# Optimization experiments

Hardware: AMD Instinct MI355X
Metric: run time of the kernel (lower is better)

## Reference

```python
import jax, jax.numpy as jnp
import numpy as np

TAU = 0.05
EPS = 1e-12


def _l2_normalize(x):
    # F.normalize(p=2): x / max(||x||, eps)
    n = jnp.sqrt(jnp.sum(x * x, axis=-1, keepdims=True))
    return x / jnp.maximum(n, EPS)


def _masked_lse(sim, mask):
    # logsumexp over axis -1 restricted to mask; rows with empty mask are
    # masked out downstream (has_pos), so we guard the log to stay finite.
    neg_inf = jnp.finfo(sim.dtype).min
    mx = jnp.max(jnp.where(mask, sim, neg_inf), axis=-1)
    mx_safe = jnp.where(mx > neg_inf / 2, mx, 0.0)
    s = jnp.sum(jnp.where(mask, jnp.exp(sim - mx_safe[:, None]), 0.0), axis=-1)
    return mx_safe + jnp.log(jnp.where(s > 0, s, 1.0))


def setup_inputs() -> dict:
    key = jax.random.key(0)
    k1, k2, k3, k4 = jax.random.split(key, 4)
    B, S, D = 64, 128, 256
    return {
        "logits": jax.random.normal(k1, (B, S, D), dtype=jnp.float32),
        "labels": jax.random.normal(k2, (B, S, D), dtype=jnp.float32),
        "pad_mask": jax.random.randint(k3, (B, S), 0, 2, dtype=jnp.int32),
        "ad_idxs": jax.random.randint(k4, (B, S), 0, 500, dtype=jnp.int32),
    }


def reference(logits, labels, pad_mask, ad_idxs):
    B, S, D = logits.shape
    q = _l2_normalize(logits.reshape(B * S, D))
    k = _l2_normalize(labels.reshape(B * S, D))
    valid = pad_mask.reshape(B * S).astype(bool)
    ad = ad_idxs.reshape(B * S)

    sim = jnp.einsum("nd,md->nm", q, k) / TAU          # [N, N]
    pair_valid = valid[None, :] & valid[:, None]
    pos_mask = (ad[None, :] == ad[:, None]) & pair_valid

    pos_lse = _masked_lse(sim, pos_mask)
    all_lse = _masked_lse(sim, pair_valid)
    has_pos = jnp.any(pos_mask, axis=-1)

    loss_per_row = -(pos_lse - all_lse)
    # mean over rows with at least one positive (== loss_per_row[has_pos].mean())
    cnt = jnp.sum(has_pos.astype(sim.dtype))
    loss = jnp.sum(jnp.where(has_pos, loss_per_row, 0.0)) / jnp.maximum(cnt, 1.0)
    return loss
```

## Files before the change

### kernel.cpp

```cpp
#include <hip/hip_runtime.h>
#include <hip/hip_bf16.h>
#include <hip/hip_fp8.h>
#include <math.h>

typedef float f32x4 __attribute__((ext_vector_type(4)));
typedef int   i32x4 __attribute__((ext_vector_type(4)));
typedef int   v8i   __attribute__((ext_vector_type(8)));

constexpr int Nn = 8192;
constexpr int Dd = 256;
constexpr float LOG2E     = 1.4426950408889634f;
constexpr float SIM_SCALE = 20.0f * LOG2E;
constexpr float SIM_BIAS  = -20.0f * LOG2E;
constexpr int   SCALE1    = 0x7F7F7F7F;

typedef __attribute__((address_space(1))) const unsigned int gu32;
typedef __attribute__((address_space(3))) unsigned int lu32;
__device__ __forceinline__ void gload16(const unsigned char* g, unsigned char* l) {
  __builtin_amdgcn_global_load_lds((gu32*)(uintptr_t)g, (lu32*)(uintptr_t)l, 16, 0, 0);
}

__global__ __launch_bounds__(256) void prep_kernel(const float* __restrict__ logits,
                                                   const float* __restrict__ labels,
                                                   const int* __restrict__ pad,
                                                   unsigned char* __restrict__ qb,
                                                   unsigned char* __restrict__ kb,
                                                   float* __restrict__ cbias,
                                                   float* __restrict__ g_all,
                                                   float* __restrict__ g_pos) {
  const int j = blockIdx.x * 256 + threadIdx.x;
  if (j < Nn) {
    cbias[j] = pad[j] ? SIM_BIAS : -1e30f;
    g_all[j] = 0.0f;
    g_pos[j] = 0.0f;
  }

  const int gw   = (blockIdx.x * 256 + threadIdx.x) >> 6;
  const int lane = threadIdx.x & 63;
  const float* src;
  unsigned char* dst;
  int row;
  if (gw < Nn) { src = logits; dst = qb; row = gw; }
  else         { src = labels; dst = kb; row = gw - Nn; }

  const float4 v = *reinterpret_cast<const float4*>(src + (size_t)row * Dd + lane * 4);
  float ss = v.x * v.x + v.y * v.y + v.z * v.z + v.w * v.w;
#pragma unroll
  for (int m = 32; m >= 1; m >>= 1) ss += __shfl_xor(ss, m);
  const float scale = 1.0f / fmaxf(sqrtf(ss), 1e-12f);

  const __hip_fp8_e4m3 e0(v.x * scale);
  const __hip_fp8_e4m3 e1(v.y * scale);
  const __hip_fp8_e4m3 e2(v.z * scale);
  const __hip_fp8_e4m3 e3(v.w * scale);
  const unsigned int packed = (unsigned int)e0.__x |
                              ((unsigned int)e1.__x << 8) |
                              ((unsigned int)e2.__x << 16) |
                              ((unsigned int)e3.__x << 24);
  reinterpret_cast<unsigned int*>(dst + (size_t)row * Dd)[lane] = packed;
}

__global__ __launch_bounds__(256, 2) void gemm_lse_kernel(const unsigned char* __restrict__ qb,
                                                          const unsigned char* __restrict__ kb,
                                                          const float* __restrict__ cbias,
                                                          const int* __restrict__ ad,
                                                          float* __restrict__ g_all,
                                                          float* __restrict__ g_pos) {
  __shared__ unsigned char smem[65536];

  const int tid  = threadIdx.x;
  const int lane = tid & 63;
  const int w    = tid >> 6;
  const int wrow = (w >> 1) * 64;
  const int wcolL = (w & 1) * 64;
  const int lq   = lane & 15;
  const int qd   = lane >> 4;
  const int rowBase = blockIdx.x * 128;
  const int colBase = blockIdx.y * 1024;

  const int srl = lane >> 3;
  const int cg  = (lane & 7) ^ srl;
  const unsigned char* gA0 = qb + (size_t)(rowBase + w * 32 + srl) * Dd + cg * 16;
  const unsigned char* gB0 = kb + (size_t)(colBase + w * 32 + srl) * Dd + cg * 16;

#pragma unroll
  for (int kk = 0; kk < 2; ++kk)
#pragma unroll
    for (int i = 0; i < 4; ++i)
      gload16(gA0 + (size_t)i * 8 * Dd + kk * 128,
              &smem[kk * 16384 + (w * 32 + i * 8) * 128]);
#pragma unroll
  for (int i = 0; i < 4; ++i)
    gload16(gB0 + (size_t)i * 8 * Dd, &smem[32768 + (w * 32 + i * 8) * 128]);

  int rowAd[4][4];
#pragma unroll
  for (int mt = 0; mt < 4; ++mt)
#pragma unroll
    for (int r = 0; r < 4; ++r)
      rowAd[mt][r] = ad[rowBase + wrow + mt * 16 + qd * 4 + r];

  float apA[4][4], apP[4][4];
#pragma unroll
  for (int mt = 0; mt < 4; ++mt)
#pragma unroll
    for (int r = 0; r < 4; ++r) {
      apA[mt][r] = 0.f;
      apP[mt][r] = 0.f;
    }

  __syncthreads();

  const int g0 = qd << 1;
  const int sl = lq & 7;
  const int s0 = (g0 ^ sl) << 4;
  const int s1 = ((g0 + 1) ^ sl) << 4;

  v8i afReg[2][4];
#pragma unroll
  for (int kk = 0; kk < 2; ++kk) {
    const unsigned char* Ah = &smem[kk * 16384];
#pragma unroll
    for (int mt = 0; mt < 4; ++mt) {
      const int rb = (wrow + mt * 16 + lq) * 128;
      i32x4* ph = reinterpret_cast<i32x4*>(&afReg[kk][mt]);
      ph[0] = *reinterpret_cast<const i32x4*>(&Ah[rb + s0]);
      ph[1] = *reinterpret_cast<const i32x4*>(&Ah[rb + s1]);
    }
  }

  const f32x4 CZ = (f32x4){0.f, 0.f, 0.f, 0.f};
  f32x4 c[4][4];
  float colB[4];
  int colAd[4];

  for (int ct = 0; ct < 8; ++ct) {
    {
      const unsigned char* g = gB0 + (size_t)(ct * 128) * Dd + 128;
      unsigned char* dB = &smem[32768 + 16384 + (w * 32) * 128];
#pragma unroll
      for (int i = 0; i < 4; ++i)
        gload16(g + (size_t)i * 8 * Dd, dB + i * 8 * 128);

#pragma unroll
      for (int nt = 0; nt < 4; ++nt) {
        const int col = colBase + ct * 128 + wcolL + nt * 16 + lq;
        colB[nt]  = cbias[col];
        colAd[nt] = ad[col];
      }

      const unsigned char* Bh = &smem[32768];
#pragma unroll
      for (int nt = 0; nt < 4; ++nt) {
        const int rb = (wcolL + nt * 16 + lq) * 128;
        v8i bf;
        i32x4* pb = reinterpret_cast<i32x4*>(&bf);
        pb[0] = *reinterpret_cast<const i32x4*>(&Bh[rb + s0]);
        pb[1] = *reinterpret_cast<const i32x4*>(&Bh[rb + s1]);
#pragma unroll
        for (int mt = 0; mt < 4; ++mt)
          c[mt][nt] = __builtin_amdgcn_mfma_scale_f32_16x16x128_f8f6f4(
              afReg[0][mt], bf, CZ, 0, 0, 0, SCALE1, 0, SCALE1);
      }
      __syncthreads();
    }

    {
      if (ct < 7) {
        const unsigned char* g = gB0 + (size_t)((ct + 1) * 128) * Dd;
        unsigned char* dB = &smem[32768 + (w * 32) * 128];
#pragma unroll
        for (int i = 0; i < 4; ++i)
          gload16(g + (size_t)i * 8 * Dd, dB + i * 8 * 128);
      }

      const unsigned char* Bh = &smem[32768 + 16384];
#pragma unroll
      for (int nt = 0; nt < 4; ++nt) {
        const int rb = (wcolL + nt * 16 + lq) * 128;
        v8i bf;
        i32x4* pb = reinterpret_cast<i32x4*>(&bf);
        pb[0] = *reinterpret_cast<const i32x4*>(&Bh[rb + s0]);
        pb[1] = *reinterpret_cast<const i32x4*>(&Bh[rb + s1]);
#pragma unroll
        for (int mt = 0; mt < 4; ++mt)
          c[mt][nt] = __builtin_amdgcn_mfma_scale_f32_16x16x128_f8f6f4(
              afReg[1][mt], bf, c[mt][nt], 0, 0, 0, SCALE1, 0, SCALE1);
      }

#pragma unroll
      for (int mt = 0; mt < 4; ++mt) {
#pragma unroll
        for (int r = 0; r < 4; ++r) {
          float a = 0.f, p = 0.f;
#pragma unroll
          for (int nt = 0; nt < 4; ++nt) {
            const float e = __builtin_amdgcn_exp2f(fmaf(c[mt][nt][r], SIM_SCALE, colB[nt]));
            a += e;
            p += (colAd[nt] == rowAd[mt][r]) ? e : 0.f;
          }
          apA[mt][r] += a;
          apP[mt][r] += p;
        }
      }
      __syncthreads();
    }
  }

#pragma unroll
  for (int mt = 0; mt < 4; ++mt) {
#pragma unroll
    for (int r = 0; r < 4; ++r) {
      float a = apA[mt][r], p = apP[mt][r];
#pragma unroll
      for (int m = 1; m < 16; m <<= 1) {
        a += __shfl_xor(a, m);
        p += __shfl_xor(p, m);
      }
      if (lq == 0) {
        const int row = rowBase + wrow + mt * 16 + qd * 4 + r;
        atomicAdd(&g_all[row], a);
        atomicAdd(&g_pos[row], p);
      }
    }
  }
}

__global__ __launch_bounds__(1024) void reduce_kernel(const float* __restrict__ g_all,
                                                      const float* __restrict__ g_pos,
                                                      const int* __restrict__ pad,
                                                      float* __restrict__ out) {
  __shared__ float sS[16], sC[16];
  const int t = threadIdx.x;
  float s = 0.f, c = 0.f;
  const float4* ga4 = (const float4*)g_all;
  const float4* gp4 = (const float4*)g_pos;
  const int4*   pd4 = (const int4*)pad;
  for (int i = t; i < Nn / 4; i += 1024) {
    const float4 ga = ga4[i];
    const float4 gp = gp4[i];
    const int4   pd = pd4[i];
    if (pd.x) { s += __logf(ga.x) - __logf(gp.x); c += 1.f; }
    if (pd.y) { s += __logf(ga.y) - __logf(gp.y); c += 1.f; }
    if (pd.z) { s += __logf(ga.z) - __logf(gp.z); c += 1.f; }
    if (pd.w) { s += __logf(ga.w) - __logf(gp.w); c += 1.f; }
  }
#pragma unroll
  for (int m = 32; m >= 1; m >>= 1) {
    s += __shfl_xor(s, m);
    c += __shfl_xor(c, m);
  }
  if ((t & 63) == 0) { sS[t >> 6] = s; sC[t >> 6] = c; }
  __syncthreads();
  if (t == 0) {
    float S = 0.f, C = 0.f;
#pragma unroll
    for (int i = 0; i < 16; ++i) { S += sS[i]; C += sC[i]; }
    out[0] = S / fmaxf(C, 1.0f);
  }
}

extern "C" void kernel_launch(void* const* d_in, const int* in_sizes, int n_in,
                              void* d_out, int out_size, void* d_ws, size_t ws_size,
                              hipStream_t stream) {
  const float* logits = (const float*)d_in[0];
  const float* labels = (const float*)d_in[1];
  const int*   pad    = (const int*)d_in[2];
  const int*   ad     = (const int*)d_in[3];

  char* ws = (char*)d_ws;
  unsigned char* qb = (unsigned char*)(ws);
  unsigned char* kb = (unsigned char*)(ws + 2097152);
  float*  cb   = (float*)(ws + 4194304);
  float*  gAll = (float*)(ws + 4227072);
  float*  gPos = (float*)(ws + 4259840);
  float*  out  = (float*)d_out;

  prep_kernel<<<4096, 256, 0, stream>>>(logits, labels, pad, qb, kb, cb, gAll, gPos);
  gemm_lse_kernel<<<dim3(64, 8), 256, 0, stream>>>(qb, kb, cb, ad, gAll, gPos);
  reduce_kernel<<<1, 1024, 0, stream>>>(gAll, gPos, pad, out);
}
```

Before: 102.2 us.

## Use triple-buffered B tiles with explicit vmcnt waits and reuse A smem

Shrinks shared memory from 64KB to 48KB by reusing the A staging area as one of three rotating B half-tile buffers after A is loaded into registers. Replaces __syncthreads with explicit s_waitcnt vmcnt/lgkmcnt plus raw barriers, so one prefetch can stay in flight while the current half-tile is consumed. The aim is better overlap of global-to-LDS loads with MFMA work and possibly higher occupancy. The cost is fragile hand-managed wait counts and buffer rotation logic that must line up exactly with the number of outstanding loads.

```diff
diff --git a/kernel.cpp b/kernel.cpp
--- a/kernel.cpp
+++ b/kernel.cpp
@@ -19,6 +19,12 @@
 __device__ __forceinline__ void gload16(const unsigned char* g, unsigned char* l) {
   __builtin_amdgcn_global_load_lds((gu32*)(uintptr_t)g, (lu32*)(uintptr_t)l, 16, 0, 0);
 }
+
+#define VMCNT4() asm volatile("s_waitcnt vmcnt(4)" ::: "memory")
+#define VMCNT0() asm volatile("s_waitcnt vmcnt(0)" ::: "memory")
+#define LGKM0()  asm volatile("s_waitcnt lgkmcnt(0)" ::: "memory")
+#define SCHEDB() __builtin_amdgcn_sched_barrier(0)
+#define BAR()    __builtin_amdgcn_s_barrier()
 
 __global__ __launch_bounds__(256) void prep_kernel(const float* __restrict__ logits,
                                                    const float* __restrict__ labels,
@@ -66,12 +72,12 @@
                                                           const int* __restrict__ ad,
                                                           float* __restrict__ g_all,
                                                           float* __restrict__ g_pos) {
-  __shared__ unsigned char smem[65536];
+  __shared__ unsigned char smem[49152];
 
   const int tid  = threadIdx.x;
   const int lane = tid & 63;
   const int w    = tid >> 6;
-  const int wrow = (w >> 1) * 64;
+  const int wrow  = (w >> 1) * 64;
   const int wcolL = (w & 1) * 64;
   const int lq   = lane & 15;
   const int qd   = lane >> 4;
@@ -109,12 +115,12 @@
       apP[mt][r] = 0.f;
     }
 
-  __syncthreads();
-
-  const int g0 = qd << 1;
+  VMCNT4();
+  BAR();
+
   const int sl = lq & 7;
-  const int s0 = (g0 ^ sl) << 4;
-  const int s1 = ((g0 + 1) ^ sl) << 4;
+  const int s0 = ((qd * 2) ^ sl) << 4;
+  const int s1 = ((qd * 2 + 1) ^ sl) << 4;
 
   v8i afReg[2][4];
 #pragma unroll
@@ -123,10 +129,20 @@
 #pragma unroll
     for (int mt = 0; mt < 4; ++mt) {
       const int rb = (wrow + mt * 16 + lq) * 128;
-      i32x4* ph = reinterpret_cast<i32x4*>(&afReg[kk][mt]);
-      ph[0] = *reinterpret_cast<const i32x4*>(&Ah[rb + s0]);
-      ph[1] = *reinterpret_cast<const i32x4*>(&Ah[rb + s1]);
-    }
+      i32x4* ph_ = reinterpret_cast<i32x4*>(&afReg[kk][mt]);
+      ph_[0] = *reinterpret_cast<const i32x4*>(&Ah[rb + s0]);
+      ph_[1] = *reinterpret_cast<const i32x4*>(&Ah[rb + s1]);
+    }
+  }
+
+  __syncthreads();
+
+  {
+    unsigned char* dB = &smem[0 + (w * 32) * 128];
+    const unsigned char* g = gB0 + 128;
+#pragma unroll
+    for (int i = 0; i < 4; ++i)
+      gload16(g + (size_t)i * 8 * Dd, dB + i * 8 * 128);
   }
 
   const f32x4 CZ = (f32x4){0.f, 0.f, 0.f, 0.f};
@@ -135,12 +151,15 @@
   int colAd[4];
 
   for (int ct = 0; ct < 8; ++ct) {
+    const int sA = (2 * ct) % 3;
+    const unsigned bas0 = (sA == 0) ? 32768u : ((sA == 1) ? 0u : 16384u);
+    const unsigned bas1 = (sA == 2) ? 32768u : ((sA == 0) ? 0u : 16384u);
+    const unsigned bas2 = (sA == 1) ? 32768u : ((sA == 2) ? 0u : 16384u);
+    const unsigned bas3 = bas0;
+
     {
-      const unsigned char* g = gB0 + (size_t)(ct * 128) * Dd + 128;
-      unsigned char* dB = &smem[32768 + 16384 + (w * 32) * 128];
-#pragma unroll
-      for (int i = 0; i < 4; ++i)
-        gload16(g + (size_t)i * 8 * Dd, dB + i * 8 * 128);
+      VMCNT4();
+      BAR();
 
 #pragma unroll
       for (int nt = 0; nt < 4; ++nt) {
@@ -149,7 +168,15 @@
         colAd[nt] = ad[col];
       }
 
-      const unsigned char* Bh = &smem[32768];
+      if (ct < 7) {
+        unsigned char* dB = &smem[bas2 + (w * 32) * 128];
+        const unsigned char* g = gB0 + (size_t)((ct + 1) * 128) * Dd;
+#pragma unroll
+        for (int i = 0; i < 4; ++i)
+          gload16(g + (size_t)i * 8 * Dd, dB + i * 8 * 128);
+      }
+
+      const unsigned char* Bh = &smem[bas0];
 #pragma unroll
       for (int nt = 0; nt < 4; ++nt) {
         const int rb = (wcolL + nt * 16 + lq) * 128;
@@ -162,19 +189,23 @@
           c[mt][nt] = __builtin_amdgcn_mfma_scale_f32_16x16x128_f8f6f4(
               afReg[0][mt], bf, CZ, 0, 0, 0, SCALE1, 0, SCALE1);
       }
-      __syncthreads();
+      LGKM0();
+      SCHEDB();
     }
 
     {
+      if (ct < 7) { VMCNT4(); } else { VMCNT0(); }
+      BAR();
+
       if (ct < 7) {
-        const unsigned char* g = gB0 + (size_t)((ct + 1) * 128) * Dd;
-        unsigned char* dB = &smem[32768 + (w * 32) * 128];
+        unsigned char* dB = &smem[bas3 + (w * 32) * 128];
+        const unsigned char* g = gB0 + (size_t)((ct + 1) * 128) * Dd + 128;
 #pragma unroll
         for (int i = 0; i < 4; ++i)
           gload16(g + (size_t)i * 8 * Dd, dB + i * 8 * 128);
       }
 
-      const unsigned char* Bh = &smem[32768 + 16384];
+      const unsigned char* Bh = &smem[bas1];
 #pragma unroll
       for (int nt = 0; nt < 4; ++nt) {
         const int rb = (wcolL + nt * 16 + lq) * 128;
@@ -187,6 +218,8 @@
           c[mt][nt] = __builtin_amdgcn_mfma_scale_f32_16x16x128_f8f6f4(
               afReg[1][mt], bf, c[mt][nt], 0, 0, 0, SCALE1, 0, SCALE1);
       }
+      LGKM0();
+      SCHEDB();
 
 #pragma unroll
       for (int mt = 0; mt < 4; ++mt) {
@@ -203,7 +236,6 @@
           apP[mt][r] += p;
         }
       }
-      __syncthreads();
     }
   }
 
```

After: 100.1 us. -2.0%, faster.

## Shrink GEMM tiles to 64 rows and add triple-buffered B pipeline with explicit waitcnts

Applied to the files above, without the earlier changes.

Halves the row tile per block (64 rows, 1024 columns in 64-column steps), doubling the grid to 1024 blocks and cutting LDS to 40 KB so four blocks can fit per CU. Replaces the double-buffered B staging and full __syncthreads with a three-slot ring of async global-to-LDS loads, gated by explicit vmcnt/lgkmcnt waits and raw s_barrier. The aim is better occupancy and overlap of B loads with MFMA and exp work. In exchange each block does less compute per barrier, reloads B tiles twice as often across row blocks, and relies on hand-counted vmcnt values that could race if miscounted.

```diff
diff --git a/kernel.cpp b/kernel.cpp
--- a/kernel.cpp
+++ b/kernel.cpp
@@ -19,6 +19,13 @@
 __device__ __forceinline__ void gload16(const unsigned char* g, unsigned char* l) {
   __builtin_amdgcn_global_load_lds((gu32*)(uintptr_t)g, (lu32*)(uintptr_t)l, 16, 0, 0);
 }
+
+#define VMCNT2() asm volatile("s_waitcnt vmcnt(2)" ::: "memory")
+#define VMCNT6() asm volatile("s_waitcnt vmcnt(6)" ::: "memory")
+#define VMCNT0() asm volatile("s_waitcnt vmcnt(0)" ::: "memory")
+#define LGKM0()  asm volatile("s_waitcnt lgkmcnt(0)" ::: "memory")
+#define SCHEDB() __builtin_amdgcn_sched_barrier(0)
+#define BAR()    __builtin_amdgcn_s_barrier()
 
 __global__ __launch_bounds__(256) void prep_kernel(const float* __restrict__ logits,
                                                    const float* __restrict__ labels,
@@ -60,155 +67,154 @@
   reinterpret_cast<unsigned int*>(dst + (size_t)row * Dd)[lane] = packed;
 }
 
-__global__ __launch_bounds__(256, 2) void gemm_lse_kernel(const unsigned char* __restrict__ qb,
+__global__ __launch_bounds__(256, 4) void gemm_lse_kernel(const unsigned char* __restrict__ qb,
                                                           const unsigned char* __restrict__ kb,
                                                           const float* __restrict__ cbias,
                                                           const int* __restrict__ ad,
                                                           float* __restrict__ g_all,
                                                           float* __restrict__ g_pos) {
-  __shared__ unsigned char smem[65536];
+  __shared__ unsigned char smem[40960];
 
   const int tid  = threadIdx.x;
   const int lane = tid & 63;
   const int w    = tid >> 6;
-  const int wrow = (w >> 1) * 64;
-  const int wcolL = (w & 1) * 64;
+  const int wr   = w >> 1;
+  const int wc   = w & 1;
   const int lq   = lane & 15;
   const int qd   = lane >> 4;
-  const int rowBase = blockIdx.x * 128;
+  const int rowBase = blockIdx.x * 64;
   const int colBase = blockIdx.y * 1024;
 
-  const int srl = lane >> 3;
-  const int cg  = (lane & 7) ^ srl;
-  const unsigned char* gA0 = qb + (size_t)(rowBase + w * 32 + srl) * Dd + cg * 16;
-  const unsigned char* gB0 = kb + (size_t)(colBase + w * 32 + srl) * Dd + cg * 16;
-
-#pragma unroll
-  for (int kk = 0; kk < 2; ++kk)
-#pragma unroll
-    for (int i = 0; i < 4; ++i)
-      gload16(gA0 + (size_t)i * 8 * Dd + kk * 128,
-              &smem[kk * 16384 + (w * 32 + i * 8) * 128]);
+  const unsigned char* gA = qb + (size_t)(rowBase + w * 16 + (lane >> 4)) * Dd
+                               + (((lane & 15) ^ (lane >> 4)) << 4);
 #pragma unroll
   for (int i = 0; i < 4; ++i)
-    gload16(gB0 + (size_t)i * 8 * Dd, &smem[32768 + (w * 32 + i * 8) * 128]);
-
-  int rowAd[4][4];
-#pragma unroll
-  for (int mt = 0; mt < 4; ++mt)
+    gload16(gA + i * 1024, &smem[w * 4096 + i * 1024]);
+
+  const unsigned char* gB = kb + (size_t)(colBase + w * 16 + (lane >> 3)) * Dd
+                               + (((lane & 7) ^ (lane >> 3)) << 4);
+
+#define STAGE_B(t, slot) do {                                         \
+    unsigned char* dB_ = &smem[16384 + (slot) * 8192 + w * 2048];     \
+    const unsigned char* gS_ = gB + ((t) >> 1) * 16384 + ((t) & 1) * 128; \
+    gload16(gS_,        dB_);                                         \
+    gload16(gS_ + 2048, dB_ + 1024);                                  \
+  } while (0)
+
+  STAGE_B(0, 0);
+
+  int rowAd[2][4];
+#pragma unroll
+  for (int mt = 0; mt < 2; ++mt)
 #pragma unroll
     for (int r = 0; r < 4; ++r)
-      rowAd[mt][r] = ad[rowBase + wrow + mt * 16 + qd * 4 + r];
-
-  float apA[4][4], apP[4][4];
-#pragma unroll
-  for (int mt = 0; mt < 4; ++mt)
+      rowAd[mt][r] = ad[rowBase + wr * 32 + mt * 16 + qd * 4 + r];
+
+  float apA[2][4], apP[2][4];
+#pragma unroll
+  for (int mt = 0; mt < 2; ++mt)
 #pragma unroll
     for (int r = 0; r < 4; ++r) {
       apA[mt][r] = 0.f;
       apP[mt][r] = 0.f;
     }
 
-  __syncthreads();
-
-  const int g0 = qd << 1;
-  const int sl = lq & 7;
-  const int s0 = (g0 ^ sl) << 4;
-  const int s1 = ((g0 + 1) ^ sl) << 4;
-
-  v8i afReg[2][4];
-#pragma unroll
-  for (int kk = 0; kk < 2; ++kk) {
-    const unsigned char* Ah = &smem[kk * 16384];
-#pragma unroll
-    for (int mt = 0; mt < 4; ++mt) {
-      const int rb = (wrow + mt * 16 + lq) * 128;
-      i32x4* ph = reinterpret_cast<i32x4*>(&afReg[kk][mt]);
-      ph[0] = *reinterpret_cast<const i32x4*>(&Ah[rb + s0]);
-      ph[1] = *reinterpret_cast<const i32x4*>(&Ah[rb + s1]);
-    }
-  }
-
+  VMCNT2();
+  BAR();
+
+  v8i afReg[2][2];
+#pragma unroll
+  for (int kk = 0; kk < 2; ++kk)
+#pragma unroll
+    for (int mt = 0; mt < 2; ++mt) {
+      const int row = wr * 32 + mt * 16 + lq;
+      const int gg  = kk * 8 + qd * 2;
+      i32x4* ph_ = reinterpret_cast<i32x4*>(&afReg[kk][mt]);
+      ph_[0] = *reinterpret_cast<const i32x4*>(&smem[row * 256 + ((gg ^ (lq & 3)) << 4)]);
+      ph_[1] = *reinterpret_cast<const i32x4*>(&smem[row * 256 + (((gg + 1) ^ (lq & 3)) << 4)]);
+    }
+  STAGE_B(1, 1);
+
+  const int s0 = ((qd * 2) ^ (lq & 7)) << 4;
+  const int s1 = ((qd * 2 + 1) ^ (lq & 7)) << 4;
   const f32x4 CZ = (f32x4){0.f, 0.f, 0.f, 0.f};
-  f32x4 c[4][4];
-  float colB[4];
-  int colAd[4];
-
-  for (int ct = 0; ct < 8; ++ct) {
+
+  for (int ct = 0; ct < 16; ++ct) {
+    const int b0 = (2 * ct) % 3;
+    const int b1 = (2 * ct + 1) % 3;
+    const int b2 = (2 * ct + 2) % 3;
+    f32x4 c[2][2];
+    float colB[2];
+    int colAd[2];
+
+    VMCNT2();
+    BAR();
+#pragma unroll
+    for (int nt = 0; nt < 2; ++nt) {
+      const int col = colBase + ct * 64 + wc * 32 + nt * 16 + lq;
+      colB[nt]  = cbias[col];
+      colAd[nt] = ad[col];
+    }
+    if (ct < 15) STAGE_B(2 * ct + 2, b2);
     {
-      const unsigned char* g = gB0 + (size_t)(ct * 128) * Dd + 128;
-      unsigned char* dB = &smem[32768 + 16384 + (w * 32) * 128];
-#pragma unroll
-      for (int i = 0; i < 4; ++i)
-        gload16(g + (size_t)i * 8 * Dd, dB + i * 8 * 128);
-
-#pragma unroll
-      for (int nt = 0; nt < 4; ++nt) {
-        const int col = colBase + ct * 128 + wcolL + nt * 16 + lq;
-        colB[nt]  = cbias[col];
-        colAd[nt] = ad[col];
-      }
-
-      const unsigned char* Bh = &smem[32768];
-#pragma unroll
-      for (int nt = 0; nt < 4; ++nt) {
-        const int rb = (wcolL + nt * 16 + lq) * 128;
+      const unsigned char* Bh = &smem[16384 + b0 * 8192];
+#pragma unroll
+      for (int nt = 0; nt < 2; ++nt) {
+        const int rb = (wc * 32 + nt * 16 + lq) * 128;
         v8i bf;
         i32x4* pb = reinterpret_cast<i32x4*>(&bf);
         pb[0] = *reinterpret_cast<const i32x4*>(&Bh[rb + s0]);
         pb[1] = *reinterpret_cast<const i32x4*>(&Bh[rb + s1]);
 #pragma unroll
-        for (int mt = 0; mt < 4; ++mt)
+        for (int mt = 0; mt < 2; ++mt)
           c[mt][nt] = __builtin_amdgcn_mfma_scale_f32_16x16x128_f8f6f4(
               afReg[0][mt], bf, CZ, 0, 0, 0, SCALE1, 0, SCALE1);
       }
-      __syncthreads();
-    }
-
+    }
+    LGKM0();
+    SCHEDB();
+
+    if (ct < 15) { VMCNT6(); } else { VMCNT0(); }
+    BAR();
+    if (ct < 15) STAGE_B(2 * ct + 3, b0);
     {
-      if (ct < 7) {
-        const unsigned char* g = gB0 + (size_t)((ct + 1) * 128) * Dd;
-        unsigned char* dB = &smem[32768 + (w * 32) * 128];
-#pragma unroll
-        for (int i = 0; i < 4; ++i)
-          gload16(g + (size_t)i * 8 * Dd, dB + i * 8 * 128);
-      }
-
-      const unsigned char* Bh = &smem[32768 + 16384];
-#pragma unroll
-      for (int nt = 0; nt < 4; ++nt) {
-        const int rb = (wcolL + nt * 16 + lq) * 128;
+      const unsigned char* Bh = &smem[16384 + b1 * 8192];
+#pragma unroll
+      for (int nt = 0; nt < 2; ++nt) {
+        const int rb = (wc * 32 + nt * 16 + lq) * 128;
         v8i bf;
         i32x4* pb = reinterpret_cast<i32x4*>(&bf);
         pb[0] = *reinterpret_cast<const i32x4*>(&Bh[rb + s0]);
         pb[1] = *reinterpret_cast<const i32x4*>(&Bh[rb + s1]);
 #pragma unroll
-        for (int mt = 0; mt < 4; ++mt)
+        for (int mt = 0; mt < 2; ++mt)
           c[mt][nt] = __builtin_amdgcn_mfma_scale_f32_16x16x128_f8f6f4(
               afReg[1][mt], bf, c[mt][nt], 0, 0, 0, SCALE1, 0, SCALE1);
       }
-
-#pragma unroll
-      for (int mt = 0; mt < 4; ++mt) {
-#pragma unroll
-        for (int r = 0; r < 4; ++r) {
-          float a = 0.f, p = 0.f;
-#pragma unroll
-          for (int nt = 0; nt < 4; ++nt) {
-            const float e = __builtin_amdgcn_exp2f(fmaf(c[mt][nt][r], SIM_SCALE, colB[nt]));
-            a += e;
-            p += (colAd[nt] == rowAd[mt][r]) ? e : 0.f;
-          }
-          apA[mt][r] += a;
-          apP[mt][r] += p;
+    }
+    LGKM0();
+    SCHEDB();
+
+#pragma unroll
+    for (int mt = 0; mt < 2; ++mt) {
+#pragma unroll
+      for (int r = 0; r < 4; ++r) {
+        float a = 0.f, p = 0.f;
+#pragma unroll
+        for (int nt = 0; nt < 2; ++nt) {
+          const float e = __builtin_amdgcn_exp2f(fmaf(c[mt][nt][r], SIM_SCALE, colB[nt]));
+          a += e;
+          p += (colAd[nt] == rowAd[mt][r]) ? e : 0.f;
         }
-      }
-      __syncthreads();
-    }
-  }
-
-#pragma unroll
-  for (int mt = 0; mt < 4; ++mt) {
+        apA[mt][r] += a;
+        apP[mt][r] += p;
+      }
+    }
+  }
+#undef STAGE_B
+
+#pragma unroll
+  for (int mt = 0; mt < 2; ++mt) {
 #pragma unroll
     for (int r = 0; r < 4; ++r) {
       float a = apA[mt][r], p = apP[mt][r];
@@ -218,7 +224,7 @@
         p += __shfl_xor(p, m);
       }
       if (lq == 0) {
-        const int row = rowBase + wrow + mt * 16 + qd * 4 + r;
+        const int row = rowBase + wr * 32 + mt * 16 + qd * 4 + r;
         atomicAdd(&g_all[row], a);
         atomicAdd(&g_pos[row], p);
       }
@@ -277,6 +283,6 @@
   float*  out  = (float*)d_out;
 
   prep_kernel<<<4096, 256, 0, stream>>>(logits, labels, pad, qb, kb, cb, gAll, gPos);
-  gemm_lse_kernel<<<dim3(64, 8), 256, 0, stream>>>(qb, kb, cb, ad, gAll, gPos);
+  gemm_lse_kernel<<<dim3(128, 8), 256, 0, stream>>>(qb, kb, cb, ad, gAll, gPos);
   reduce_kernel<<<1, 1024, 0, stream>>>(gAll, gPos, pad, out);
 }
```

New measurement: 101.8 us. About the same (-0.4%).
